# Optimization experiments

Hardware: AMD Instinct MI355X
Metric: run time of the kernel (lower is better)

The kernel has to match this reference:

```python
import jax, jax.numpy as jnp
import numpy as np

TIME_WINDOW = 80
TC_IN = 17.452274
TD = 0.0
TC1 = TC2 = TC3 = 20.0
V_INIT = 1.0
NOT_FIRED = 9999.0


def setup_inputs() -> dict:
    key = jax.random.key(0)
    k0, k1, k2, k3, k4, k5, k6 = jax.random.split(key, 7)
    B = 4096
    return {
        "input_image": jax.random.uniform(k0, (B, 1, 28, 28), dtype=jnp.float32),
        "conv1_w": jax.random.normal(k1, (12, 1, 5, 5), dtype=jnp.float32) * 0.3,
        "conv1_b": jax.random.normal(k2, (12,), dtype=jnp.float32) * 0.1,
        "conv2_w": jax.random.normal(k3, (64, 12, 5, 5), dtype=jnp.float32) * 0.1,
        "conv2_b": jax.random.normal(k4, (64,), dtype=jnp.float32) * 0.1,
        "fc1_w": jax.random.normal(k5, (1024, 10), dtype=jnp.float32) * 0.1,
        "fc1_b": jax.random.normal(k6, (10,), dtype=jnp.float32) * 0.1,
    }


def _conv(x, w, b):
    y = jax.lax.conv_general_dilated(x, w, (1, 1), "VALID",
                                     dimension_numbers=("NCHW", "OIHW", "NCHW"))
    return y + b[None, :, None, None]


def _max_pool2x2(x):
    return jax.lax.reduce_window(x, -jnp.inf, jax.lax.max,
                                 (1, 1, 2, 2), (1, 1, 2, 2), "VALID")


def _neuron(v_mem, has_fired, curr, t, tc):
    # TemporalNeuron: integrate, dynamic threshold v_init*exp(-(t-td)/tc), fire once.
    v_mem = v_mem + curr
    v_th = V_INIT * jnp.exp(-(t - TD) / tc)
    fire = (v_mem >= v_th) & (~has_fired) & (v_th > 1e-5)
    return v_mem, has_fired | fire, fire.astype(v_mem.dtype)


def _ttfs_pool(x, fired_mask):
    # Min-time pooling: only the earliest spike in each 2x2 window passes.
    p = _max_pool2x2(x)
    valid = (p > 0.5) & (~fired_mask)
    return valid.astype(x.dtype), fired_mask | valid


def reference(input_image, conv1_w, conv1_b, conv2_w, conv2_b, fc1_w, fc1_b):
    B = input_image.shape[0]
    # Inputs are in [0,1) so no /255 branch (pixel.max() <= 1.05 in original).
    pixel = jnp.clip(input_image, 1e-5, None)
    spike_times_in = jnp.ceil(jnp.clip(-TC_IN * jnp.log(pixel), 0.0, None))

    init = (
        jnp.zeros((B, 12, 24, 24), jnp.float32), jnp.zeros((B, 12, 24, 24), bool),
        jnp.zeros((B, 12, 12, 12), bool),
        jnp.zeros((B, 64, 8, 8), jnp.float32), jnp.zeros((B, 64, 8, 8), bool),
        jnp.zeros((B, 64, 4, 4), bool),
        jnp.zeros((B, 10), jnp.float32), jnp.zeros((B, 10), bool),
        jnp.full((B, 10), NOT_FIRED, jnp.float32),
    )

    def step(carry, t):
        v1, f1, pm1, v2, f2, pm2, v3, f3, out_times = carry
        mask_in = (jnp.abs(t - spike_times_in) < 0.5).astype(jnp.float32)
        v1, f1, spk1 = _neuron(v1, f1, _conv(mask_in, conv1_w, conv1_b), t, TC1)
        spk1_p, pm1 = _ttfs_pool(spk1, pm1)
        v2, f2, spk2 = _neuron(v2, f2, _conv(spk1_p, conv2_w, conv2_b), t, TC2)
        spk2_p, pm2 = _ttfs_pool(spk2, pm2)
        flat = spk2_p.transpose(0, 2, 3, 1).reshape(B, -1)  # NHWC flatten, matches torch permute
        v3, f3, spk3 = _neuron(v3, f3, flat @ fc1_w + fc1_b, t, TC3)
        out_times = jnp.where((spk3 > 0.5) & (out_times == NOT_FIRED), t, out_times)
        return (v1, f1, pm1, v2, f2, pm2, v3, f3, out_times), None

    ts = jnp.arange(TIME_WINDOW, dtype=jnp.float32)
    carry, _ = jax.lax.scan(step, init, ts)
    return carry[-1]
```

## Files before the change

kernel.cpp:

```cpp
#include <hip/hip_runtime.h>
#include <math.h>

#define NOT_FIREDf 9999.0f
typedef float f32x2 __attribute__((ext_vector_type(2)));

#define PKADD(ACC, W) asm("v_pk_add_f32 %0, %0, %1" : "+v"(ACC) : "v"(W))

__global__ void w2_pad_kernel(const float* __restrict__ w2, float* __restrict__ w2p) {
    int idx = blockIdx.x * 256 + threadIdx.x;
    if (idx >= 74176) return;
    if (idx >= 72960) { w2p[idx] = 0.0f; return; }
    int co = idx & 63;
    int r = idx >> 6;
    int rx = r % 19;
    int q = r / 19;
    int dy = q % 5;
    int ci = q / 5;
    int dx = rx - 7;
    w2p[idx] = ((unsigned)dx < 5u) ? w2[(co * 12 + ci) * 25 + dy * 5 + dx] : 0.0f;
}

#define GATHER_V1(S, Y, X) do {                                              \
    const int dy_ = py - (Y), dx_ = px - (X);                                \
    if (((unsigned)dy_ < 5u) & ((unsigned)dx_ < 5u)) {                       \
        const f32x2* wp_ = (const f32x2*)&w1s[(dy_ * 5 + dx_) * 12];         \
        PKADD(v1r[S][0], wp_[0]); PKADD(v1r[S][1], wp_[1]);                  \
        PKADD(v1r[S][2], wp_[2]); PKADD(v1r[S][3], wp_[3]);                  \
        PKADD(v1r[S][4], wp_[4]); PKADD(v1r[S][5], wp_[5]);                  \
    } } while (0)

#define P1EVENT(PK) do {                                                     \
    const int py = (int)((PK) >> 8);                                         \
    const int px = (int)((PK) & 255u);                                       \
    GATHER_V1(0, y0, x0);                                                    \
    GATHER_V1(1, y1, x1);                                                    \
    if (has2) GATHER_V1(2, y2, x2);                                          \
  } while (0)

#define CHECK_V1G(S, Y, X) do {                                              \
    const f32x2* bp_ = (const f32x2*)b1s;                                    \
    PKADD(v1r[S][0], bp_[0]); PKADD(v1r[S][1], bp_[1]);                      \
    PKADD(v1r[S][2], bp_[2]); PKADD(v1r[S][3], bp_[3]);                      \
    PKADD(v1r[S][4], bp_[4]); PKADD(v1r[S][5], bp_[5]);                      \
    float m_ = fmaxf(fmaxf(fmaxf(v1r[S][0].x, v1r[S][0].y),                  \
                           fmaxf(v1r[S][1].x, v1r[S][1].y)),                 \
                     fmaxf(fmaxf(v1r[S][2].x, v1r[S][2].y),                  \
                           fmaxf(v1r[S][3].x, v1r[S][3].y)));                \
    m_ = fmaxf(m_, fmaxf(fmaxf(v1r[S][4].x, v1r[S][4].y),                    \
                         fmaxf(v1r[S][5].x, v1r[S][5].y)));                  \
    if (m_ >= th) {                                                          \
        _Pragma("unroll")                                                    \
        for (int jj = 0; jj < 6; ++jj) {                                     \
            _Pragma("unroll")                                                \
            for (int el = 0; el < 2; ++el) {                                 \
                const float v_ = el ? v1r[S][jj].y : v1r[S][jj].x;           \
                if (v_ >= th) {                                              \
                    if (el) v1r[S][jj].y = -__builtin_inff();                \
                    else    v1r[S][jj].x = -__builtin_inff();                \
                    const int c_ = jj * 2 + el;                              \
                    const int pyp_ = (Y) >> 1, pxp_ = (X) >> 1;              \
                    const int p_ = c_ * 144 + pyp_ * 12 + pxp_;              \
                    const unsigned bit_ = 1u << (p_ & 31);                   \
                    const unsigned old_ = atomicOr(&pm1[p_ >> 5], bit_);     \
                    if (!(old_ & bit_)) {                                    \
                        const int pos_ = atomicAdd(&cnt1[t], 1);             \
                        ev1b[t & 1][pos_] =                                  \
                            (unsigned short)((c_ << 8) | (pyp_ << 4) | pxp_);\
                    }                                                        \
                }                                                            \
            }                                                                \
        }                                                                    \
    } } while (0)

#define P2_ONE(PA) do {                                                      \
    const int dA_ = (((PA) >> 4) & 15) - oyb_s;                              \
    if ((unsigned)dA_ < 6u) {                                                \
        const int ci_ = (PA) >> 8;                                           \
        const int px_ = (PA) & 15;                                           \
        const float* r0_ = (dA_ <= 4) ? (w2p + (ci_ * 5 + dA_) * 1216) : zrow; \
        const float* r1_ = (dA_ >= 1) ? (w2p + (ci_ * 5 + dA_ - 1) * 1216) : zrow; \
        const float* q0_ = r0_ + (px_ + 7) * 64 + lane;                      \
        const float* q1_ = r1_ + (px_ + 7) * 64 + lane;                      \
        f32x2 la_[4];                                                        \
        _Pragma("unroll")                                                    \
        for (int j = 0; j < 4; ++j) { la_[j].x = q0_[-(j * 64)]; la_[j].y = q1_[-(j * 64)]; } \
        _Pragma("unroll")                                                    \
        for (int j = 0; j < 4; ++j) PKADD(v2r2[j], la_[j]);                  \
        _Pragma("unroll")                                                    \
        for (int j = 0; j < 4; ++j) { la_[j].x = q0_[-((4 + j) * 64)]; la_[j].y = q1_[-((4 + j) * 64)]; } \
        _Pragma("unroll")                                                    \
        for (int j = 0; j < 4; ++j) PKADD(v2r2[4 + j], la_[j]);              \
    } } while (0)

template <int USE_T>
__global__ void __launch_bounds__(256, 4)
snn_sim_kernel(const float* __restrict__ img,
               const float* __restrict__ w1g,
               const float* __restrict__ b1g,
               const float* __restrict__ b2g,
               const float* __restrict__ w2raw,
               const float* __restrict__ w2p,
               const float* __restrict__ fcw,
               const float* __restrict__ b3g,
               float* __restrict__ out) {
    const int bimg = blockIdx.x;
    const int tid  = threadIdx.x;
    const int lane = tid & 63;
    const int wv   = tid >> 6;
    const int oyb_s = __builtin_amdgcn_readfirstlane(wv) * 2;

    __shared__ __align__(16) float w1s[300];
    __shared__ __align__(8)  float b1s[12];
    __shared__ float th_lds[80];
    __shared__ unsigned char  stin[784];
    __shared__ unsigned short evlist[784];
    __shared__ unsigned short off[81];
    __shared__ unsigned int   hist[80];
    __shared__ __align__(8) unsigned short ev1b[2][1728];
    __shared__ int            cnt1[80];
    __shared__ unsigned int   pm1[54];
    __shared__ unsigned int   pm2[32];
    __shared__ unsigned int   e2list[1024];
    __shared__ int            e2_cnt;

    for (int i = tid; i < 300; i += 256) {
        int k = i / 12, c = i - k * 12;
        w1s[i] = w1g[c * 25 + k];
    }
    if (tid < 12) b1s[tid] = b1g[tid];
    if (tid < 80) {
        float xa = (0.0f - (float)tid) / 20.0f;
        th_lds[tid] = (float)exp((double)xa);
        hist[tid] = 0u;
        cnt1[tid] = 0;
    }
    if (tid < 54) pm1[tid] = 0u;
    if (tid < 32) pm2[tid] = 0u;
    if (tid == 0) e2_cnt = 0;
    for (int i = tid; i < 784; i += 256) {
        float p = img[bimg * 784 + i];
        p = fmaxf(p, 1e-5f);
        float lg = (float)log((double)p);
        float s = ceilf(fmaxf(-17.452274f * lg, 0.0f));
        stin[i] = (unsigned char)(int)fminf(s, 255.0f);
    }
    __syncthreads();
    for (int i = tid; i < 784; i += 256) {
        int t = stin[i];
        if (t < 80) atomicAdd(&hist[t], 1u);
    }
    __syncthreads();
    if (tid == 0) {
        unsigned int acc = 0;
        for (int t = 0; t < 80; ++t) { off[t] = (unsigned short)acc; acc += hist[t]; }
        off[80] = (unsigned short)acc;
    }
    __syncthreads();
    if (tid < 80) {
        int k = off[tid];
        for (int i = 0; i < 784; ++i)
            if ((int)stin[i] == tid) {
                int py = i / 28;
                evlist[k++] = (unsigned short)((py << 8) | (i - py * 28));
            }
    }
    __syncthreads();

    f32x2 v1r[3][6];
#pragma unroll
    for (int s = 0; s < 3; ++s)
#pragma unroll
        for (int j = 0; j < 6; ++j) v1r[s][j] = (f32x2){0.0f, 0.0f};
    f32x2 v2r2[8];
#pragma unroll
    for (int j = 0; j < 8; ++j) v2r2[j] = (f32x2){0.0f, 0.0f};

    const float b2v = b2g[lane];
    const f32x2 b2p = (f32x2){b2v, b2v};
    const float* zrow = w2p + 72960;

    const int y0 = tid / 24,  x0 = tid - y0 * 24;
    const int p1i = tid + 256;
    const int y1 = p1i / 24,  x1 = p1i - y1 * 24;
    const int has2 = (tid < 64);
    const int p2i = tid + 512;
    const int y2 = p2i / 24,  x2 = p2i - y2 * 24;

    for (int t = 0; t < 80; ++t) {
        const float th = th_lds[t];

        {
            const int e0 = off[t], e1t = off[t + 1];
            int e = e0;
            for (; e + 4 <= e1t; e += 4) {
                const unsigned a0 = evlist[e];
                const unsigned a1 = evlist[e + 1];
                const unsigned a2 = evlist[e + 2];
                const unsigned a3 = evlist[e + 3];
                P1EVENT(a0); P1EVENT(a1); P1EVENT(a2); P1EVENT(a3);
            }
            for (; e < e1t; ++e) { const unsigned a = evlist[e]; P1EVENT(a); }
        }
        CHECK_V1G(0, y0, x0);
        CHECK_V1G(1, y1, x1);
        if (has2) CHECK_V1G(2, y2, x2);
        __syncthreads();

        {
            const int ne1 = cnt1[t];
            const unsigned short* evp = ev1b[t & 1];
            if (USE_T) {
                int e = 0;
                for (; e + 4 <= ne1; e += 4) {
                    const unsigned long long pk4 = *(const unsigned long long*)&evp[e];
                    const unsigned lo = (unsigned)__builtin_amdgcn_readfirstlane((int)(unsigned)pk4);
                    const unsigned hi = (unsigned)__builtin_amdgcn_readfirstlane((int)(unsigned)(pk4 >> 32));
                    const int p0 = (int)(lo & 0xFFFFu), p1 = (int)(lo >> 16);
                    const int p2 = (int)(hi & 0xFFFFu), p3 = (int)(hi >> 16);
                    P2_ONE(p0); P2_ONE(p1); P2_ONE(p2); P2_ONE(p3);
                }
                for (; e < ne1; ++e) {
                    const int p0 = __builtin_amdgcn_readfirstlane((int)evp[e]);
                    P2_ONE(p0);
                }
            } else {
                for (int e = 0; e < ne1; ++e) {
                    const int pk = __builtin_amdgcn_readfirstlane((int)evp[e]);
                    const int dy0 = ((pk >> 4) & 15) - oyb_s;
                    if ((unsigned)dy0 >= 6u) continue;
                    const int ci = pk >> 8;
                    const int px = pk & 15;
                    const int dy1 = dy0 - 1;
                    const unsigned colm = ((0x1Fu << px) >> 4) & 0xFFu;
                    const unsigned m0 = ((unsigned)dy0 < 5u) ? colm : 0u;
                    const unsigned m1 = ((unsigned)dy1 < 5u) ? colm : 0u;
                    const int dy0c = dy0 < 0 ? 0 : (dy0 > 4 ? 4 : dy0);
                    const int dy1c = dy1 < 0 ? 0 : (dy1 > 4 ? 4 : dy1);
                    const float* cb = w2raw + lane * 300 + ci * 25;
                    const float* r0 = cb + dy0c * 5;
                    const float* r1 = cb + dy1c * 5;
#pragma unroll
                    for (int j = 0; j < 8; ++j) {
                        const int dx = px - j;
                        const int dxc = dx < 0 ? 0 : (dx > 4 ? 4 : dx);
                        v2r2[j].x = fmaf(r0[dxc], ((m0 >> j) & 1u) ? 1.0f : 0.0f, v2r2[j].x);
                        v2r2[j].y = fmaf(r1[dxc], ((m1 >> j) & 1u) ? 1.0f : 0.0f, v2r2[j].y);
                    }
                }
            }
        }
        {
            PKADD(v2r2[0], b2p); PKADD(v2r2[1], b2p);
            PKADD(v2r2[2], b2p); PKADD(v2r2[3], b2p);
            PKADD(v2r2[4], b2p); PKADD(v2r2[5], b2p);
            PKADD(v2r2[6], b2p); PKADD(v2r2[7], b2p);
            float m2 = fmaxf(fmaxf(fmaxf(v2r2[0].x, v2r2[0].y), fmaxf(v2r2[1].x, v2r2[1].y)),
                             fmaxf(fmaxf(v2r2[2].x, v2r2[2].y), fmaxf(v2r2[3].x, v2r2[3].y)));
            m2 = fmaxf(m2, fmaxf(fmaxf(fmaxf(v2r2[4].x, v2r2[4].y), fmaxf(v2r2[5].x, v2r2[5].y)),
                                 fmaxf(fmaxf(v2r2[6].x, v2r2[6].y), fmaxf(v2r2[7].x, v2r2[7].y))));
            if (m2 >= th) {
#pragma unroll
                for (int j = 0; j < 8; ++j) {
#pragma unroll
                    for (int el = 0; el < 2; ++el) {
                        const float v = el ? v2r2[j].y : v2r2[j].x;
                        if (v >= th) {
                            if (el) v2r2[j].y = -__builtin_inff();
                            else    v2r2[j].x = -__builtin_inff();
                            const int oy = oyb_s + el;
                            const int p2 = ((oy >> 1) * 4 + (j >> 1)) * 64 + lane;
                            const unsigned bit = 1u << (p2 & 31);
                            const unsigned old = atomicOr(&pm2[p2 >> 5], bit);
                            if (!(old & bit)) {
                                const int pos = atomicAdd(&e2_cnt, 1);
                                e2list[pos] = ((unsigned)t << 16) | (unsigned)p2;
                            }
                        }
                    }
                }
            }
        }
    }
    __syncthreads();

    if (tid < 10) {
        const int n2 = e2_cnt;
        const float b3v = b3g[tid];
        float v = 0.0f;
        float ot = NOT_FIREDf;
        int ptr = 0;
        for (int t = 0; t < 80; ++t) {
            float acc = 0.0f;
            while (ptr < n2 && (int)(e2list[ptr] >> 16) == t) {
                acc += fcw[(e2list[ptr] & 0xFFFFu) * 10 + tid];
                ++ptr;
            }
            v += acc + b3v;
            if (ot == NOT_FIREDf && v >= th_lds[t]) ot = (float)t;
        }
        out[bimg * 10 + tid] = ot;
    }
}

extern "C" void kernel_launch(void* const* d_in, const int* in_sizes, int n_in,
                              void* d_out, int out_size, void* d_ws, size_t ws_size,
                              hipStream_t stream) {
    const float* img = (const float*)d_in[0];
    const float* w1  = (const float*)d_in[1];
    const float* b1  = (const float*)d_in[2];
    const float* w2  = (const float*)d_in[3];
    const float* b2  = (const float*)d_in[4];
    const float* fcw = (const float*)d_in[5];
    const float* b3  = (const float*)d_in[6];
    float* out = (float*)d_out;

    const int B = in_sizes[0] / (28 * 28);

    float* w2p = (float*)d_ws;
    const int use_t = (ws_size >= 74176u * sizeof(float)) ? 1 : 0;
    if (use_t) {
        hipLaunchKernelGGL(w2_pad_kernel, dim3(290), dim3(256), 0, stream, w2, w2p);
        hipLaunchKernelGGL(snn_sim_kernel<1>, dim3(B), dim3(256), 0, stream,
                           img, w1, b1, b2, w2, w2p, fcw, b3, out);
    } else {
        hipLaunchKernelGGL(snn_sim_kernel<0>, dim3(B), dim3(256), 0, stream,
                           img, w1, b1, b2, w2, w2p, fcw, b3, out);
    }
}
```

Baseline: 3.247 ms.

## Decouple conv1 and conv2 time loops via per-neuron fire-time tables

Runs all 80 timesteps of layer 1 first, recording each conv1 neuron's fire time in a byte table, then derives pooled-spike times with a min over each 2x2 window. Those are bucketed into a time-sorted event list by histogram and prefix sum, and layer 2 runs its own 80-step loop over that list. This removes the per-timestep __syncthreads and the LDS atomicOr/atomicAdd pooling bookkeeping, and layer-2 pooling becomes a per-thread register bitmask. It adds serial 80-thread scans over 1728 and 1024 entries to build the sorted lists, which may cost more than the syncs it removes.

```diff
diff --git a/kernel.cpp b/kernel.cpp
--- a/kernel.cpp
+++ b/kernel.cpp
@@ -37,7 +37,7 @@
     if (has2) GATHER_V1(2, y2, x2);                                          \
   } while (0)
 
-#define CHECK_V1G(S, Y, X) do {                                              \
+#define CHECK_V1F(S, Y, X) do {                                              \
     const f32x2* bp_ = (const f32x2*)b1s;                                    \
     PKADD(v1r[S][0], bp_[0]); PKADD(v1r[S][1], bp_[1]);                      \
     PKADD(v1r[S][2], bp_[2]); PKADD(v1r[S][3], bp_[3]);                      \
@@ -59,14 +59,9 @@
                     else    v1r[S][jj].x = -__builtin_inff();                \
                     const int c_ = jj * 2 + el;                              \
                     const int pyp_ = (Y) >> 1, pxp_ = (X) >> 1;              \
-                    const int p_ = c_ * 144 + pyp_ * 12 + pxp_;              \
-                    const unsigned bit_ = 1u << (p_ & 31);                   \
-                    const unsigned old_ = atomicOr(&pm1[p_ >> 5], bit_);     \
-                    if (!(old_ & bit_)) {                                    \
-                        const int pos_ = atomicAdd(&cnt1[t], 1);             \
-                        ev1b[t & 1][pos_] =                                  \
-                            (unsigned short)((c_ << 8) | (pyp_ << 4) | pxp_);\
-                    }                                                        \
+                    const int bidx_ = ((c_ * 144 + pyp_ * 12 + pxp_) << 2)   \
+                                    | (((Y) & 1) << 1) | ((X) & 1);          \
+                    f1b[bidx_] = (unsigned char)t;                           \
                 }                                                            \
             }                                                                \
         }                                                                    \
@@ -91,6 +86,13 @@
         _Pragma("unroll")                                                    \
         for (int j = 0; j < 4; ++j) PKADD(v2r2[4 + j], la_[j]);              \
     } } while (0)
+
+__device__ __forceinline__ unsigned min4b(unsigned w) {
+    unsigned a = w & 255u, b = (w >> 8) & 255u, c = (w >> 16) & 255u, d = w >> 24;
+    unsigned m0 = a < b ? a : b;
+    unsigned m1 = c < d ? c : d;
+    return m0 < m1 ? m0 : m1;
+}
 
 template <int USE_T>
 __global__ void __launch_bounds__(256, 4)
@@ -108,6 +110,7 @@
     const int lane = tid & 63;
     const int wv   = tid >> 6;
     const int oyb_s = __builtin_amdgcn_readfirstlane(wv) * 2;
+    const int wv_s  = oyb_s >> 1;
 
     __shared__ __align__(16) float w1s[300];
     __shared__ __align__(8)  float b1s[12];
@@ -115,13 +118,13 @@
     __shared__ unsigned char  stin[784];
     __shared__ unsigned short evlist[784];
     __shared__ unsigned short off[81];
+    __shared__ unsigned short o1[81];
     __shared__ unsigned int   hist[80];
-    __shared__ __align__(8) unsigned short ev1b[2][1728];
-    __shared__ int            cnt1[80];
-    __shared__ unsigned int   pm1[54];
-    __shared__ unsigned int   pm2[32];
-    __shared__ unsigned int   e2list[1024];
-    __shared__ int            e2_cnt;
+    __shared__ unsigned int   f1w[1728];
+    __shared__ __align__(8) unsigned short ev1s[1728];
+    __shared__ unsigned char  e2t[1024];
+
+    unsigned char* f1b = (unsigned char*)f1w;
 
     for (int i = tid; i < 300; i += 256) {
         int k = i / 12, c = i - k * 12;
@@ -132,11 +135,9 @@
         float xa = (0.0f - (float)tid) / 20.0f;
         th_lds[tid] = (float)exp((double)xa);
         hist[tid] = 0u;
-        cnt1[tid] = 0;
-    }
-    if (tid < 54) pm1[tid] = 0u;
-    if (tid < 32) pm2[tid] = 0u;
-    if (tid == 0) e2_cnt = 0;
+    }
+    for (int i = tid; i < 1728; i += 256) f1w[i] = 0xFFFFFFFFu;
+    for (int i = tid; i < 1024; i += 256) e2t[i] = 0xFF;
     for (int i = tid; i < 784; i += 256) {
         float p = img[bimg * 784 + i];
         p = fmaxf(p, 1e-5f);
@@ -164,32 +165,25 @@
                 evlist[k++] = (unsigned short)((py << 8) | (i - py * 28));
             }
     }
-    __syncthreads();
-
-    f32x2 v1r[3][6];
-#pragma unroll
-    for (int s = 0; s < 3; ++s)
-#pragma unroll
-        for (int j = 0; j < 6; ++j) v1r[s][j] = (f32x2){0.0f, 0.0f};
-    f32x2 v2r2[8];
-#pragma unroll
-    for (int j = 0; j < 8; ++j) v2r2[j] = (f32x2){0.0f, 0.0f};
-
-    const float b2v = b2g[lane];
-    const f32x2 b2p = (f32x2){b2v, b2v};
-    const float* zrow = w2p + 72960;
-
-    const int y0 = tid / 24,  x0 = tid - y0 * 24;
-    const int p1i = tid + 256;
-    const int y1 = p1i / 24,  x1 = p1i - y1 * 24;
-    const int has2 = (tid < 64);
-    const int p2i = tid + 512;
-    const int y2 = p2i / 24,  x2 = p2i - y2 * 24;
-
-    for (int t = 0; t < 80; ++t) {
-        const float th = th_lds[t];
-
-        {
+    if (tid >= 80 && tid < 160) hist[tid - 80] = 0u;
+    __syncthreads();
+
+    {
+        f32x2 v1r[3][6];
+#pragma unroll
+        for (int s = 0; s < 3; ++s)
+#pragma unroll
+            for (int j = 0; j < 6; ++j) v1r[s][j] = (f32x2){0.0f, 0.0f};
+
+        const int y0 = tid / 24,  x0 = tid - y0 * 24;
+        const int p1i = tid + 256;
+        const int y1 = p1i / 24,  x1 = p1i - y1 * 24;
+        const int has2 = (tid < 64);
+        const int p2i = tid + 512;
+        const int y2 = p2i / 24,  x2 = p2i - y2 * 24;
+
+        for (int t = 0; t < 80; ++t) {
+            const float th = th_lds[t];
             const int e0 = off[t], e1t = off[t + 1];
             int e = e0;
             for (; e + 4 <= e1t; e += 4) {
@@ -200,32 +194,67 @@
                 P1EVENT(a0); P1EVENT(a1); P1EVENT(a2); P1EVENT(a3);
             }
             for (; e < e1t; ++e) { const unsigned a = evlist[e]; P1EVENT(a); }
+            CHECK_V1F(0, y0, x0);
+            CHECK_V1F(1, y1, x1);
+            if (has2) CHECK_V1F(2, y2, x2);
         }
-        CHECK_V1G(0, y0, x0);
-        CHECK_V1G(1, y1, x1);
-        if (has2) CHECK_V1G(2, y2, x2);
-        __syncthreads();
-
-        {
-            const int ne1 = cnt1[t];
-            const unsigned short* evp = ev1b[t & 1];
+    }
+    __syncthreads();
+
+    for (int p = tid; p < 1728; p += 256) {
+        unsigned tm = min4b(f1w[p]);
+        if (tm < 80u) atomicAdd(&hist[tm], 1u);
+    }
+    __syncthreads();
+    if (tid == 0) {
+        unsigned acc = 0;
+        for (int t = 0; t < 80; ++t) { o1[t] = (unsigned short)acc; acc += hist[t]; }
+        o1[80] = (unsigned short)acc;
+    }
+    __syncthreads();
+    if (tid < 80) {
+        int k = o1[tid];
+        for (int p = 0; p < 1728; ++p) {
+            if (min4b(f1w[p]) == (unsigned)tid) {
+                int c = p / 144;
+                int rem = p - c * 144;
+                int py = rem / 12;
+                int px = rem - py * 12;
+                ev1s[k++] = (unsigned short)((c << 8) | (py << 4) | px);
+            }
+        }
+    }
+    if (tid >= 80 && tid < 160) hist[tid - 80] = 0u;
+    __syncthreads();
+
+    {
+        f32x2 v2r2[8];
+#pragma unroll
+        for (int j = 0; j < 8; ++j) v2r2[j] = (f32x2){0.0f, 0.0f};
+        const float b2v = b2g[lane];
+        const f32x2 b2p = (f32x2){b2v, b2v};
+        const float* zrow = w2p + 72960;
+        unsigned fired2 = 0u;
+
+        for (int t = 0; t < 80; ++t) {
+            const float th = th_lds[t];
+            const int e0 = o1[t], e1t = o1[t + 1];
             if (USE_T) {
-                int e = 0;
-                for (; e + 4 <= ne1; e += 4) {
-                    const unsigned long long pk4 = *(const unsigned long long*)&evp[e];
-                    const unsigned lo = (unsigned)__builtin_amdgcn_readfirstlane((int)(unsigned)pk4);
-                    const unsigned hi = (unsigned)__builtin_amdgcn_readfirstlane((int)(unsigned)(pk4 >> 32));
-                    const int p0 = (int)(lo & 0xFFFFu), p1 = (int)(lo >> 16);
-                    const int p2 = (int)(hi & 0xFFFFu), p3 = (int)(hi >> 16);
+                int e = e0;
+                for (; e + 4 <= e1t; e += 4) {
+                    const int p0 = __builtin_amdgcn_readfirstlane((int)ev1s[e]);
+                    const int p1 = __builtin_amdgcn_readfirstlane((int)ev1s[e + 1]);
+                    const int p2 = __builtin_amdgcn_readfirstlane((int)ev1s[e + 2]);
+                    const int p3 = __builtin_amdgcn_readfirstlane((int)ev1s[e + 3]);
                     P2_ONE(p0); P2_ONE(p1); P2_ONE(p2); P2_ONE(p3);
                 }
-                for (; e < ne1; ++e) {
-                    const int p0 = __builtin_amdgcn_readfirstlane((int)evp[e]);
+                for (; e < e1t; ++e) {
+                    const int p0 = __builtin_amdgcn_readfirstlane((int)ev1s[e]);
                     P2_ONE(p0);
                 }
             } else {
-                for (int e = 0; e < ne1; ++e) {
-                    const int pk = __builtin_amdgcn_readfirstlane((int)evp[e]);
+                for (int e = e0; e < e1t; ++e) {
+                    const int pk = __builtin_amdgcn_readfirstlane((int)ev1s[e]);
                     const int dy0 = ((pk >> 4) & 15) - oyb_s;
                     if ((unsigned)dy0 >= 6u) continue;
                     const int ci = pk >> 8;
@@ -248,8 +277,6 @@
                     }
                 }
             }
-        }
-        {
             PKADD(v2r2[0], b2p); PKADD(v2r2[1], b2p);
             PKADD(v2r2[2], b2p); PKADD(v2r2[3], b2p);
             PKADD(v2r2[4], b2p); PKADD(v2r2[5], b2p);
@@ -267,13 +294,11 @@
                         if (v >= th) {
                             if (el) v2r2[j].y = -__builtin_inff();
                             else    v2r2[j].x = -__builtin_inff();
-                            const int oy = oyb_s + el;
-                            const int p2 = ((oy >> 1) * 4 + (j >> 1)) * 64 + lane;
-                            const unsigned bit = 1u << (p2 & 31);
-                            const unsigned old = atomicOr(&pm2[p2 >> 5], bit);
-                            if (!(old & bit)) {
-                                const int pos = atomicAdd(&e2_cnt, 1);
-                                e2list[pos] = ((unsigned)t << 16) | (unsigned)p2;
+                            const unsigned bit = 1u << (j >> 1);
+                            if (!(fired2 & bit)) {
+                                fired2 |= bit;
+                                const int p2 = (wv_s * 4 + (j >> 1)) * 64 + lane;
+                                e2t[p2] = (unsigned char)t;
                             }
                         }
                     }
@@ -283,18 +308,32 @@
     }
     __syncthreads();
 
+    for (int p = tid; p < 1024; p += 256) {
+        unsigned t = e2t[p];
+        if (t < 80u) atomicAdd(&hist[t], 1u);
+    }
+    __syncthreads();
+    if (tid == 0) {
+        unsigned acc = 0;
+        for (int t = 0; t < 80; ++t) { off[t] = (unsigned short)acc; acc += hist[t]; }
+        off[80] = (unsigned short)acc;
+    }
+    __syncthreads();
+    if (tid < 80) {
+        int k = off[tid];
+        for (int p = 0; p < 1024; ++p)
+            if ((int)e2t[p] == tid) ev1s[k++] = (unsigned short)p;
+    }
+    __syncthreads();
+
     if (tid < 10) {
-        const int n2 = e2_cnt;
         const float b3v = b3g[tid];
         float v = 0.0f;
         float ot = NOT_FIREDf;
-        int ptr = 0;
         for (int t = 0; t < 80; ++t) {
             float acc = 0.0f;
-            while (ptr < n2 && (int)(e2list[ptr] >> 16) == t) {
-                acc += fcw[(e2list[ptr] & 0xFFFFu) * 10 + tid];
-                ++ptr;
-            }
+            for (int e = off[t]; e < off[t + 1]; ++e)
+                acc += fcw[(int)ev1s[e] * 10 + tid];
             v += acc + b3v;
             if (ot == NOT_FIREDf && v >= th_lds[t]) ot = (float)t;
         }
```

Measured after the change: 2.873 ms. -11.5%, faster.
